# Kernel tuning notes

Measured on AMD Instinct MI355X. Metric: run time of the kernel, lower is better.

Reference implementation:

```python
import jax, jax.numpy as jnp
import numpy as np

BOND_TOL = 0.4
CLASH_TOL = 1.5
IDEAL_CA_CA = 3.8
EPS = 1e-08


def setup_inputs() -> dict:
    key = jax.random.key(0)
    k1, _ = jax.random.split(key)
    B, L = 8, 2048
    positions = jax.random.normal(k1, (B, L, 3), dtype=jnp.float32) * 10.0
    mask = jnp.ones((B, L), dtype=jnp.float32)
    return {"positions": positions, "mask": mask}


def reference(positions, mask):
    # positions: [B, L, 3] CA coordinates; mask: [B, L]
    L = positions.shape[1]
    ca = positions
    ca_mask = mask

    # --- bond term: consecutive CA-CA distances ---
    ca_diff = ca[:, 1:] - ca[:, :-1]                       # [B, L-1, 3]
    ca_dist = jnp.sqrt(jnp.sum(ca_diff ** 2, axis=-1) + EPS)
    bond_violation = jax.nn.relu(jnp.abs(ca_dist - IDEAL_CA_CA) - BOND_TOL)
    bond_mask = ca_mask[:, 1:] * ca_mask[:, :-1]
    bond_loss = jnp.sum(bond_violation * bond_mask) / (jnp.sum(bond_mask) + EPS)

    # --- clash term: all-pairs distances, non-bonded (|i-j| > 2) ---
    all_diff = ca[:, :, None, :] - ca[:, None, :, :]       # [B, L, L, 3]
    all_dist = jnp.sqrt(jnp.sum(all_diff ** 2, axis=-1) + EPS)  # [B, L, L]
    idx = jnp.arange(L)
    seq_sep = jnp.abs(idx[None, :] - idx[:, None])         # [L, L]
    non_bonded = (seq_sep > 2).astype(ca.dtype)
    clash_violation = jax.nn.relu(CLASH_TOL - all_dist)
    pair_mask = ca_mask[:, :, None] * ca_mask[:, None, :] * non_bonded[None]
    clash_loss = jnp.sum(clash_violation * pair_mask) / (jnp.sum(pair_mask) + EPS)

    total = bond_loss + clash_loss
    # stacked: [bond_loss, clash_loss, total_violation]
    return jnp.stack([bond_loss, clash_loss, total])
```

## Files before the change

### kernel.cpp

```cpp
#include <hip/hip_runtime.h>

#define TPB 256
#define RPB 16
#define SEQ_L 2048
#define JPT (SEQ_L / TPB)
#define NBATCH 8
#define NBLOCKS (NBATCH * (SEQ_L / RPB))

static constexpr float kBondTol  = 0.4f;
static constexpr float kClashTol = 1.5f;
static constexpr float kIdeal    = 3.8f;
static constexpr float kEps      = 1e-8f;
static constexpr float kThresh2  = 2.25f;

__device__ __forceinline__ float wred(float v) {
#pragma unroll
  for (int o = 32; o > 0; o >>= 1) v += __shfl_down(v, o, 64);
  return v;
}

__global__ __launch_bounds__(TPB, 4) void viol_main(
    const float* __restrict__ pos,
    const float* __restrict__ mask,
    float4* __restrict__ partial) {
  __shared__ float4 s[SEQ_L];
  __shared__ float  redm[TPB / 64];
  __shared__ float  red4[TPB / 64][4];

  const int blocks_per_b = SEQ_L / RPB;
  const int b  = blockIdx.x / blocks_per_b;
  const int i0 = (blockIdx.x % blocks_per_b) * RPB;
  const float* pb = pos  + (size_t)b * SEQ_L * 3;
  const float* mb = mask + (size_t)b * SEQ_L;

  float mpart = 0.f;
  for (int idx = threadIdx.x; idx < SEQ_L; idx += TPB) {
    float x = pb[3 * idx + 0];
    float y = pb[3 * idx + 1];
    float z = pb[3 * idx + 2];
    float m = mb[idx];
    s[idx] = make_float4(x, y, z, m);
    mpart += m;
  }
  mpart = wred(mpart);
  const int wid  = threadIdx.x >> 6;
  const int lane = threadIdx.x & 63;
  if (lane == 0) redm[wid] = mpart;
  __syncthreads();
  const float msum = redm[0] + redm[1] + redm[2] + redm[3];

  float px[RPB], py[RPB], pz[RPB], pw[RPB], accr[RPB];
#pragma unroll
  for (int r = 0; r < RPB; ++r) {
    float4 p = s[i0 + r];
    px[r] = p.x; py[r] = p.y; pz[r] = p.z; pw[r] = p.w;
    accr[r] = 0.f;
  }

#pragma unroll 2
  for (int k = 0; k < JPT; ++k) {
    float4 pj = s[threadIdx.x + k * TPB];
    float d2r[RPB];
    float minv;
#pragma unroll
    for (int r = 0; r < RPB; ++r) {
      float dx = pj.x - px[r];
      float dy = pj.y - py[r];
      float dz = pj.z - pz[r];
      float d2 = fmaf(dx, dx, fmaf(dy, dy, dz * dz));
      d2r[r] = d2;
      minv = (r == 0) ? d2 : fminf(minv, d2);
    }
    if (__ballot(minv < kThresh2) != 0ull) {
#pragma unroll
      for (int r = 0; r < RPB; ++r) {
        float dist = __builtin_amdgcn_sqrtf(d2r[r] + kEps);
        accr[r] = fmaf(fmaxf(kClashTol - dist, 0.f), pj.w, accr[r]);
      }
    }
  }

  float cv = 0.f, pm = 0.f, bv = 0.f, bm = 0.f;
#pragma unroll
  for (int r = 0; r < RPB; ++r) cv = fmaf(pw[r], accr[r], cv);

  if (threadIdx.x < RPB) {
    const int i = i0 + threadIdx.x;
    const float4 pi = s[i];
    float nv = 0.f, nm = 0.f;
    const int jlo = (i - 2 < 0) ? 0 : i - 2;
    const int jhi = (i + 2 > SEQ_L - 1) ? SEQ_L - 1 : i + 2;
    for (int j = jlo; j <= jhi; ++j) {
      float4 pj = s[j];
      float dx = pj.x - pi.x;
      float dy = pj.y - pi.y;
      float dz = pj.z - pi.z;
      float dist = __builtin_amdgcn_sqrtf(dx * dx + dy * dy + dz * dz + kEps);
      nv += fmaxf(kClashTol - dist, 0.f) * pj.w;
      nm += pj.w;
    }
    cv -= pi.w * nv;
    pm += pi.w * (msum - nm);

    if (i < SEQ_L - 1) {
      const float4 pj = s[i + 1];
      float dx = pj.x - pi.x;
      float dy = pj.y - pi.y;
      float dz = pj.z - pi.z;
      float dist = __builtin_amdgcn_sqrtf(dx * dx + dy * dy + dz * dz + kEps);
      float viol = fmaxf(fabsf(dist - kIdeal) - kBondTol, 0.f);
      bv += viol * pi.w * pj.w;
      bm += pi.w * pj.w;
    }
  }

  bv = wred(bv); bm = wred(bm); cv = wred(cv); pm = wred(pm);
  if (lane == 0) {
    red4[wid][0] = bv; red4[wid][1] = bm;
    red4[wid][2] = cv; red4[wid][3] = pm;
  }
  __syncthreads();
  if (threadIdx.x == 0) {
    float tbv = 0.f, tbm = 0.f, tcv = 0.f, tpm = 0.f;
#pragma unroll
    for (int w = 0; w < TPB / 64; ++w) {
      tbv += red4[w][0]; tbm += red4[w][1];
      tcv += red4[w][2]; tpm += red4[w][3];
    }
    partial[blockIdx.x] = make_float4(tbv, tbm, tcv, tpm);
  }
}

__global__ __launch_bounds__(TPB) void viol_reduce(
    const float4* __restrict__ partial, float* __restrict__ out) {
  __shared__ float red4[TPB / 64][4];
  float bv = 0.f, bm = 0.f, cv = 0.f, pm = 0.f;
#pragma unroll
  for (int i = threadIdx.x; i < NBLOCKS; i += TPB) {
    float4 p = partial[i];
    bv += p.x; bm += p.y; cv += p.z; pm += p.w;
  }
  bv = wred(bv); bm = wred(bm); cv = wred(cv); pm = wred(pm);
  const int wid  = threadIdx.x >> 6;
  const int lane = threadIdx.x & 63;
  if (lane == 0) {
    red4[wid][0] = bv; red4[wid][1] = bm;
    red4[wid][2] = cv; red4[wid][3] = pm;
  }
  __syncthreads();
  if (threadIdx.x == 0) {
    float tbv = 0.f, tbm = 0.f, tcv = 0.f, tpm = 0.f;
#pragma unroll
    for (int w = 0; w < TPB / 64; ++w) {
      tbv += red4[w][0]; tbm += red4[w][1];
      tcv += red4[w][2]; tpm += red4[w][3];
    }
    float bond  = tbv / (tbm + kEps);
    float clash = tcv / (tpm + kEps);
    out[0] = bond;
    out[1] = clash;
    out[2] = bond + clash;
  }
}

extern "C" void kernel_launch(void* const* d_in, const int* in_sizes, int n_in,
                              void* d_out, int out_size, void* d_ws, size_t ws_size,
                              hipStream_t stream) {
  const float* pos  = (const float*)d_in[0];
  const float* mask = (const float*)d_in[1];
  float* out = (float*)d_out;
  float4* partial = (float4*)d_ws;

  viol_main<<<dim3(NBLOCKS), dim3(TPB), 0, stream>>>(pos, mask, partial);
  viol_reduce<<<dim3(1), dim3(TPB), 0, stream>>>(partial, out);
}
```

Baseline: 67.16 us.

## Exploit pair symmetry to compute only upper-triangle clash pairs with balanced tiling

```diff
diff --git a/kernel.cpp b/kernel.cpp
--- a/kernel.cpp
+++ b/kernel.cpp
@@ -27,9 +27,16 @@
   __shared__ float  redm[TPB / 64];
   __shared__ float  red4[TPB / 64][4];
 
-  const int blocks_per_b = SEQ_L / RPB;
-  const int b  = blockIdx.x / blocks_per_b;
-  const int i0 = (blockIdx.x % blocks_per_b) * RPB;
+  const int u = blockIdx.x >> 3;
+  const int b = blockIdx.x & 7;
+  const int v = u >> 5, rr = u & 31;
+  int tile;
+  if      (v == 0) tile = 2 * rr;
+  else if (v == 1) tile = 127 - 2 * rr;
+  else if (v == 2) tile = 2 * rr + 1;
+  else             tile = 126 - 2 * rr;
+  const int i0 = tile << 4;
+
   const float* pb = pos  + (size_t)b * SEQ_L * 3;
   const float* mb = mask + (size_t)b * SEQ_L;
 
@@ -57,21 +64,38 @@
     accr[r] = 0.f;
   }
 
+  const int k0 = i0 >> 8;
+  {
+    const int j = threadIdx.x + (k0 << 8);
+    const float4 pj = s[j];
+#pragma unroll
+    for (int r = 0; r < RPB; ++r) {
+      const int i = i0 + r;
+      float dx = pj.x - px[r];
+      float dy = pj.y - py[r];
+      float dz = pj.z - pz[r];
+      float d2 = fmaf(dx, dx, fmaf(dy, dy, dz * dz));
+      float dist = __builtin_amdgcn_sqrtf(d2 + kEps);
+      float mw = (j > i) ? pj.w : 0.f;
+      accr[r] = fmaf(fmaxf(kClashTol - dist, 0.f), mw, accr[r]);
+    }
+  }
+
 #pragma unroll 2
-  for (int k = 0; k < JPT; ++k) {
-    float4 pj = s[threadIdx.x + k * TPB];
+  for (int k = k0 + 1; k < JPT; ++k) {
+    float4 pj = s[threadIdx.x + (k << 8)];
     float d2r[RPB];
-    float minv;
 #pragma unroll
     for (int r = 0; r < RPB; ++r) {
       float dx = pj.x - px[r];
       float dy = pj.y - py[r];
       float dz = pj.z - pz[r];
-      float d2 = fmaf(dx, dx, fmaf(dy, dy, dz * dz));
-      d2r[r] = d2;
-      minv = (r == 0) ? d2 : fminf(minv, d2);
-    }
-    if (__ballot(minv < kThresh2) != 0ull) {
+      d2r[r] = fmaf(dx, dx, fmaf(dy, dy, dz * dz));
+    }
+    float mv = d2r[0];
+#pragma unroll
+    for (int r = 1; r < RPB; ++r) mv = fminf(mv, d2r[r]);
+    if (__ballot(mv < kThresh2) != 0ull) {
 #pragma unroll
       for (int r = 0; r < RPB; ++r) {
         float dist = __builtin_amdgcn_sqrtf(d2r[r] + kEps);
@@ -87,19 +111,21 @@
   if (threadIdx.x < RPB) {
     const int i = i0 + threadIdx.x;
     const float4 pi = s[i];
-    float nv = 0.f, nm = 0.f;
-    const int jlo = (i - 2 < 0) ? 0 : i - 2;
+    float nv = 0.f;
     const int jhi = (i + 2 > SEQ_L - 1) ? SEQ_L - 1 : i + 2;
-    for (int j = jlo; j <= jhi; ++j) {
+    for (int j = i + 1; j <= jhi; ++j) {
       float4 pj = s[j];
       float dx = pj.x - pi.x;
       float dy = pj.y - pi.y;
       float dz = pj.z - pi.z;
       float dist = __builtin_amdgcn_sqrtf(dx * dx + dy * dy + dz * dz + kEps);
       nv += fmaxf(kClashTol - dist, 0.f) * pj.w;
-      nm += pj.w;
     }
     cv -= pi.w * nv;
+
+    float nm = 0.f;
+    const int jlo = (i - 2 < 0) ? 0 : i - 2;
+    for (int j = jlo; j <= jhi; ++j) nm += s[j].w;
     pm += pi.w * (msum - nm);
 
     if (i < SEQ_L - 1) {
@@ -127,7 +153,7 @@
       tbv += red4[w][0]; tbm += red4[w][1];
       tcv += red4[w][2]; tpm += red4[w][3];
     }
-    partial[blockIdx.x] = make_float4(tbv, tbm, tcv, tpm);
+    partial[blockIdx.x] = make_float4(tbv, tbm, 2.f * tcv, tpm);
   }
 }
 
```

Result: faster. 63.97 us (-4.8%).
